# Kernel optimization log

Measured on AMD Instinct MI355X. Metric: run time of the kernel, lower is better.

## Reference

```python
import jax, jax.numpy as jnp
import numpy as np

B, DX, DY = 128, 3, 3
D = DX * DY          # max_digit = 9
N = D * D            # num_nodes = 81
HID = 96
EMB = 16
ITERS = 4
M = B * N * D        # LSTM flattened rows = 93312


def _sudoku_adj():
    idx = np.arange(N)
    r, c = idx // D, idx % D
    br, bc = r // DX, c // DY
    same = (r[:, None] == r[None]) | (c[:, None] == c[None]) | ((br[:, None] == br[None]) & (bc[:, None] == bc[None]))
    return (same & ~np.eye(N, dtype=bool)).astype(np.float32)


def setup_inputs() -> dict:
    key = jax.random.key(0)
    ks = iter(jax.random.split(key, 40))

    def dense(shape, fan_in):
        return jax.random.normal(next(ks), shape, jnp.float32) / np.float32(np.sqrt(fan_in))

    return {
        "inputs": jax.random.randint(next(ks), (B, N), 0, D + 1, jnp.int32),
        "c0": jax.random.normal(next(ks), (M, HID), jnp.float32),
        "adj_cell": jnp.asarray((np.ones((D, D)) - np.eye(D)).astype(np.float32)),
        "adj_digit": jnp.asarray(_sudoku_adj()),
        "enc_W1": dense((3, EMB), 3), "enc_b1": jnp.zeros((EMB,), jnp.float32),
        "enc_W2": dense((EMB, HID), EMB), "enc_b2": jnp.zeros((HID,), jnp.float32),
        "cr_W": dense((3, HID, HID), HID), "cr_b": jnp.zeros((3, HID), jnp.float32),
        "dr_W": dense((3, HID, HID), HID), "dr_b": jnp.zeros((3, HID), jnp.float32),
        "gm_W1": dense((3 * HID, HID), 3 * HID), "gm_b1": jnp.zeros((HID,), jnp.float32),
        "gm_W2": dense((2, HID, HID), HID), "gm_b2": jnp.zeros((2, HID), jnp.float32),
        "lstm_Wih": dense((4 * HID, HID), HID), "lstm_Whh": dense((4 * HID, HID), HID),
        "lstm_bih": jnp.zeros((4 * HID,), jnp.float32), "lstm_bhh": jnp.zeros((4 * HID,), jnp.float32),
        "r_W12": dense((2, HID, HID), HID), "r_b12": jnp.zeros((2, HID), jnp.float32),
        "r_W3": dense((HID, 1), HID), "r_b3": jnp.zeros((1,), jnp.float32),
        "iters": ITERS,
    }


def _mlp(x, Ws, bs):
    # stacked MLP: ReLU between layers, none after the last
    L = Ws.shape[0]
    for l in range(L):
        x = x @ Ws[l] + bs[l]
        if l < L - 1:
            x = jax.nn.relu(x)
    return x


def _forward(inputs, c0, adj_cell, adj_digit, enc_W1, enc_b1, enc_W2, enc_b2,
             cr_W, cr_b, dr_W, dr_b, gm_W1, gm_b1, gm_W2, gm_b2,
             lstm_Wih, lstm_Whh, lstm_bih, lstm_bhh, r_W12, r_b12, r_W3, r_b3, iters):
    # mask: [B,N,D,3] = (blank, equals digit d+1, filled-with-other-digit)
    eq = inputs[:, :, None] == jnp.arange(1, D + 1, dtype=inputs.dtype)[None, None, :]
    given = inputs != 0
    mask = jnp.stack([
        jnp.broadcast_to((~given)[:, :, None], eq.shape), eq,
        (~eq) & given[:, :, None]
    ], axis=-1).astype(jnp.float32)

    X = jax.nn.relu(mask @ enc_W1 + enc_b1) @ enc_W2 + enc_b2  # [B,N,D,HID]

    def lstm_step(x, h, c):
        gates = x @ lstm_Wih.T + lstm_bih + h @ lstm_Whh.T + lstm_bhh
        i, f, g, o = jnp.split(gates, 4, axis=-1)  # PyTorch gate order i,f,g,o
        c = jax.nn.sigmoid(f) * c + jax.nn.sigmoid(i) * jnp.tanh(g)
        h = jax.nn.sigmoid(o) * jnp.tanh(c)
        return h, c

    def step(carry, _):
        h, c = carry  # [M,HID] each
        Hn = h.reshape(X.shape)
        # relational message passing: per-node MLP then sum over graph edges
        msg_cell = jnp.einsum('bndh,de->bneh', _mlp(Hn, cr_W, cr_b), adj_cell)
        msg_digit = jnp.einsum('bndh,nm->bmdh', _mlp(Hn, dr_W, dr_b), adj_digit)
        g = jnp.concatenate([X, msg_cell, msg_digit], axis=-1)  # [B,N,D,3*HID]
        g = jax.nn.relu(g @ gm_W1 + gm_b1)
        g = jax.nn.relu(g @ gm_W2[0] + gm_b2[0])
        g = g @ gm_W2[1] + gm_b2[1]
        h, c = lstm_step(g.reshape(-1, HID), h, c)
        Hn = h.reshape(X.shape)
        out = jax.nn.relu(Hn @ r_W12[0] + r_b12[0])
        out = jax.nn.relu(out @ r_W12[1] + r_b12[1])
        out = (out @ r_W3 + r_b3)[..., 0]  # [B,N,D]
        return (h, c), out

    (_, _), outs = jax.lax.scan(step, (X.reshape(-1, HID), c0), None, length=iters)
    return outs  # [iters,B,N,D]


def reference(inputs, c0, adj_cell, adj_digit, enc_W1, enc_b1, enc_W2, enc_b2,
              cr_W, cr_b, dr_W, dr_b, gm_W1, gm_b1, gm_W2, gm_b2,
              lstm_Wih, lstm_Whh, lstm_bih, lstm_bhh, r_W12, r_b12, r_W3, r_b3, iters):
    return _forward(inputs, c0, adj_cell, adj_digit, enc_W1, enc_b1, enc_W2, enc_b2,
                    cr_W, cr_b, dr_W, dr_b, gm_W1, gm_b1, gm_W2, gm_b2,
                    lstm_Wih, lstm_Whh, lstm_bih, lstm_bhh, r_W12, r_b12, r_W3, r_b3, iters)
```

## Files before the change

kernel.cpp:

```cpp
#include <hip/hip_runtime.h>
#include <hip/hip_bf16.h>

typedef unsigned short u16;
typedef __bf16 bf16x8 __attribute__((ext_vector_type(8)));
typedef float  f32x4  __attribute__((ext_vector_type(4)));
typedef u16    u16x8  __attribute__((ext_vector_type(8)));

#define HID   96
#define LDP   104
#define MROWS 93312
#define BN    10368
#define GRID_TILE 1458
#define FUSE_GRID 5832
#define SGS   104
#define PST   97

#define FCH 9216

#define MFMA(a,b,c) __builtin_amdgcn_mfma_f32_16x16x32_bf16((a),(b),(c),0,0,0)

__device__ __forceinline__ float bf2f(u16 x){
  union { float f; unsigned u; } v; v.u = ((unsigned)x) << 16; return v.f;
}
__device__ __forceinline__ u16 f2bf(float f){
  union { float f; unsigned u; } v; v.f = f;
  unsigned r = v.u + 0x7fffu + ((v.u >> 16) & 1u);
  return (u16)(r >> 16);
}
__device__ __forceinline__ float frcp(float x){ return __builtin_amdgcn_rcpf(x); }
__device__ __forceinline__ float sigf(float x){ return frcp(1.f + __expf(-x)); }
__device__ __forceinline__ float tanhf_(float x){
  float xx = fminf(fmaxf(x, -15.f), 15.f);
  float e = __expf(-2.f * xx);
  return (1.f - e) * frcp(1.f + e);
}
__device__ __forceinline__ void lds_fence(){
  asm volatile("s_waitcnt lgkmcnt(0)" ::: "memory");
}

struct Frags { bf16x8 a0, a1, a2; };

__device__ __forceinline__ Frags load_afrags_g(const u16* __restrict__ A, size_t row0, int lane){
  int t16 = lane & 15, q = lane >> 4;
  const u16* p = A + (row0 + (size_t)t16) * 96 + q * 8;
  Frags f;
  f.a0 = *reinterpret_cast<const bf16x8*>(p);
  f.a1 = *reinterpret_cast<const bf16x8*>(p + 32);
  f.a2 = *reinterpret_cast<const bf16x8*>(p + 64);
  return f;
}
__device__ __forceinline__ Frags load_afrags_s(const u16* sA, int row0, int lane){
  int t16 = lane & 15, q = lane >> 4;
  const u16* p = sA + (row0 + t16) * LDP + q * 8;
  Frags f;
  f.a0 = *reinterpret_cast<const bf16x8*>(p);
  f.a1 = *reinterpret_cast<const bf16x8*>(p + 32);
  f.a2 = *reinterpret_cast<const bf16x8*>(p + 64);
  return f;
}

__device__ __forceinline__ void layer_g(Frags f, const u16* __restrict__ wb,
    const float* __restrict__ bias, u16* dst, int dstStride, size_t rowBase,
    bool relu, int lane)
{
  int t16 = lane & 15, q = lane >> 4;
  #pragma unroll
  for (int nt = 0; nt < 6; nt++){
    float b = bias ? bias[nt * 16 + t16] : 0.f;
    f32x4 acc = {b, b, b, b};
    const u16* wp = wb + nt * 1536 + lane * 8;
    acc = MFMA(f.a0, *reinterpret_cast<const bf16x8*>(wp),        acc);
    acc = MFMA(f.a1, *reinterpret_cast<const bf16x8*>(wp + 512),  acc);
    acc = MFMA(f.a2, *reinterpret_cast<const bf16x8*>(wp + 1024), acc);
    #pragma unroll
    for (int j = 0; j < 4; j++){
      float v = acc[j];
      if (relu) v = fmaxf(v, 0.f);
      dst[(rowBase + q * 4 + j) * (size_t)dstStride + nt * 16 + t16] = f2bf(v);
    }
  }
}

__device__ __forceinline__ void layer_split(Frags f, const u16* __restrict__ wb,
    const float* __restrict__ bias, u16* dst, bool relu, int lane, int w)
{
  int t16 = lane & 15, q = lane >> 4;
  #pragma unroll
  for (int nt = w; nt < 6; nt += 4){
    float b = bias ? bias[nt * 16 + t16] : 0.f;
    f32x4 acc = {b, b, b, b};
    const u16* wp = wb + nt * 1536 + lane * 8;
    acc = MFMA(f.a0, *reinterpret_cast<const bf16x8*>(wp),        acc);
    acc = MFMA(f.a1, *reinterpret_cast<const bf16x8*>(wp + 512),  acc);
    acc = MFMA(f.a2, *reinterpret_cast<const bf16x8*>(wp + 1024), acc);
    #pragma unroll
    for (int j = 0; j < 4; j++){
      float v = acc[j];
      if (relu) v = fmaxf(v, 0.f);
      dst[(q * 4 + j) * LDP + nt * 16 + t16] = f2bf(v);
    }
  }
}

__device__ __forceinline__ void mfma6_g(f32x4* acc, Frags f,
    const u16* __restrict__ wb, int lane)
{
  #pragma unroll
  for (int jt = 0; jt < 6; jt++){
    const u16* wp = wb + jt * 1536 + lane * 8;
    acc[jt] = MFMA(f.a0, *reinterpret_cast<const bf16x8*>(wp),        acc[jt]);
    acc[jt] = MFMA(f.a1, *reinterpret_cast<const bf16x8*>(wp + 512),  acc[jt]);
    acc[jt] = MFMA(f.a2, *reinterpret_cast<const bf16x8*>(wp + 1024), acc[jt]);
  }
}

__global__ __launch_bounds__(256) void k_prep2(const float* __restrict__ crW,
    const float* __restrict__ drW, const float* __restrict__ gmW2,
    const float* __restrict__ rW12, const float* __restrict__ Whh,
    u16* __restrict__ pWB)
{
  int b = blockIdx.x, tid = threadIdx.x;
  if (b < 7){
    const float* src; int ch;
    if      (b == 0){ src = crW;          ch = 0;  }
    else if (b == 1){ src = crW  + 9216;  ch = 1;  }
    else if (b == 2){ src = drW;          ch = 3;  }
    else if (b == 3){ src = drW  + 9216;  ch = 4;  }
    else if (b == 4){ src = gmW2;         ch = 8;  }
    else if (b == 5){ src = rW12;         ch = 10; }
    else            { src = rW12 + 9216;  ch = 11; }
    u16* dst = pWB + ch * FCH;
    #pragma unroll
    for (int i = 0; i < 36; i++){
      int idx = tid + i * 256;
      int f = idx >> 9, rem = idx & 511, l = rem >> 3, j = rem & 7;
      int nt = f / 3, kc = f - nt * 3;
      int n = nt * 16 + (l & 15);
      int k = ((l >> 4) << 3) + kc * 32 + j;
      dst[idx] = f2bf(src[k * 96 + n]);
    }
  } else {
    int bb = b - 7;
    u16* dst = pWB + (16 + bb) * FCH;
    const float* src = Whh + bb * 9216;
    #pragma unroll
    for (int i = 0; i < 36; i++){
      int idx = tid + i * 256;
      int f = idx >> 9, rem = idx & 511, l = rem >> 3, j = rem & 7;
      int nt = f / 3, kc = f - nt * 3;
      int n = nt * 16 + (l & 15);
      int k = ((l >> 4) << 3) + kc * 32 + j;
      dst[idx] = f2bf(src[n * 96 + k]);
    }
  }
}

__global__ __launch_bounds__(256) void k_prepc(const float* __restrict__ crW,
    const float* __restrict__ crB, const float* __restrict__ drW,
    const float* __restrict__ drB, const float* __restrict__ gmW1,
    u16* __restrict__ pWB, float* __restrict__ bY, float* __restrict__ bZ)
{
  __shared__ float sM[96 * PST];
  __shared__ float sW[96 * PST];
  int b = blockIdx.x, g = b / 9, seg = b - g * 9, tid = threadIdx.x;
  const float* L = (g == 0 ? crW : drW) + 2 * 9216;
  const float* R = gmW1 + (g == 0 ? 9216 : 18432);
  for (int i = tid; i < 9216; i += 256){
    int r = i / 96, cc = i - r * 96;
    sM[r * PST + cc] = L[i];
    sW[r * PST + cc] = R[i];
  }
  __syncthreads();
  if (seg == 0){
    const float* bv = (g == 0 ? crB : drB) + 192;
    float* bo = (g == 0 ? bY : bZ);
    for (int n = tid; n < 96; n += 256){
      float a = 0.f;
      for (int j = 0; j < 96; j++) a += bv[j] * sW[j * PST + n];
      bo[n] = a;
    }
  }
  u16* dst = pWB + (g == 0 ? 2 : 5) * FCH;
  #pragma unroll
  for (int i = 0; i < 4; i++){
    int idx = seg * 1024 + tid + i * 256;
    int f = idx >> 9, rem = idx & 511, l = rem >> 3, j = rem & 7;
    int nt = f / 3, kc = f - nt * 3;
    int n = nt * 16 + (l & 15);
    int k = ((l >> 4) << 3) + kc * 32 + j;
    float a = 0.f;
    #pragma unroll 4
    for (int jj = 0; jj < 96; jj++) a += sM[k * PST + jj] * sW[jj * PST + n];
    dst[idx] = f2bf(a);
  }
}

__global__ __launch_bounds__(256) void k_prepf(const float* __restrict__ gmW2,
    const float* __restrict__ Wih, u16* __restrict__ pWB)
{
  __shared__ float sW[96 * PST];
  int b = blockIdx.x, g = b / 9, seg = b - g * 9, tid = threadIdx.x;
  for (int i = tid; i < 9216; i += 256){
    int r = i / 96, cc = i - r * 96;
    sW[r * PST + cc] = gmW2[9216 + i];
  }
  __syncthreads();
  u16* dst = pWB + (12 + g) * FCH;
  #pragma unroll
  for (int i = 0; i < 4; i++){
    int idx = seg * 1024 + tid + i * 256;
    int f = idx >> 9, rem = idx & 511, l = rem >> 3, j = rem & 7;
    int nt = f / 3, kc = f - nt * 3;
    int n = nt * 16 + (l & 15);
    int k = ((l >> 4) << 3) + kc * 32 + j;
    const float* wr = Wih + (g * 96 + n) * 96;
    float a = 0.f;
    #pragma unroll 4
    for (int jj = 0; jj < 96; jj++) a += sW[k * PST + jj] * wr[jj];
    dst[idx] = f2bf(a);
  }
}

__global__ void k_tables(const float* __restrict__ eW1, const float* __restrict__ eb1,
                         const float* __restrict__ eW2, const float* __restrict__ eb2,
                         const float* __restrict__ gmW1, const float* __restrict__ gmb1,
                         const float* __restrict__ bih, const float* __restrict__ bhh,
                         const float* __restrict__ gmb2, const float* __restrict__ Wih,
                         float* __restrict__ XTab, float* __restrict__ XgTab,
                         float* __restrict__ bsx)
{
  __shared__ float sX[3][96];
  int j = threadIdx.x;
  for (int n = j; n < 384; n += 128){
    float acc = bih[n] + bhh[n];
    const float* wr = Wih + n * 96;
    for (int jj = 0; jj < 96; jj++) acc += gmb2[96 + jj] * wr[jj];
    bsx[n] = acc;
  }
  if (j < 96){
    for (int ch = 0; ch < 3; ch++){
      float acc = eb2[j];
      for (int e = 0; e < 16; e++){
        float hv = fmaxf(eW1[ch * 16 + e] + eb1[e], 0.f);
        acc += hv * eW2[e * 96 + j];
      }
      sX[ch][j] = acc;
      XTab[ch * 96 + j] = acc;
    }
  }
  __syncthreads();
  if (j < 96){
    for (int ch = 0; ch < 3; ch++){
      float acc = gmb1[j];
      for (int k = 0; k < 96; k++) acc += sX[ch][k] * gmW1[k * 96 + j];
      XgTab[ch * 96 + j] = acc;
    }
  }
}

__global__ __launch_bounds__(256) void k_init(const int* __restrict__ inputs,
    const float* __restrict__ XTab, u16* __restrict__ h)
{
  int idx = blockIdx.x * 256 + threadIdx.x;
  int m = idx / 12, h8 = idx - m * 12;
  int bn = m / 9, d = m - bn * 9;
  int inp = inputs[bn];
  int ch = (inp == 0) ? 0 : ((inp == d + 1) ? 1 : 2);
  const float* xt = XTab + ch * 96 + h8 * 8;
  u16* hp = h + (size_t)m * 96 + h8 * 8;
  #pragma unroll
  for (int e = 0; e < 8; e++) hp[e] = f2bf(xt[e]);
}

__global__ __launch_bounds__(256) void k_ab3(const u16* __restrict__ h,
    u16* __restrict__ Y, u16* __restrict__ Z,
    const u16* __restrict__ pWB, const float* __restrict__ crB,
    const float* __restrict__ drB, const float* __restrict__ bY,
    const float* __restrict__ bZ)
{
  __shared__ u16 sA[64 * LDP];
  const int tid = threadIdx.x, lane = tid & 63, wave = tid >> 6;
  const int wrow = wave * 16;
  const size_t rbase = (size_t)blockIdx.x * 64;

  Frags hf = load_afrags_g(h, rbase + wrow, lane);

  layer_g(hf, pWB, crB, sA, LDP, wrow, true, lane);                  lds_fence();
  Frags f = load_afrags_s(sA, wrow, lane);
  layer_g(f, pWB + 1 * FCH, crB + 96, sA, LDP, wrow, true, lane);    lds_fence();
  f = load_afrags_s(sA, wrow, lane);
  layer_g(f, pWB + 2 * FCH, bY, Y, 96, rbase + wrow, false, lane);
  lds_fence();

  layer_g(hf, pWB + 3 * FCH, drB, sA, LDP, wrow, true, lane);        lds_fence();
  f = load_afrags_s(sA, wrow, lane);
  layer_g(f, pWB + 4 * FCH, drB + 96, sA, LDP, wrow, true, lane);    lds_fence();
  f = load_afrags_s(sA, wrow, lane);
  layer_g(f, pWB + 5 * FCH, bZ, Z, 96, rbase + wrow, false, lane);
}

__device__ __forceinline__ void addrow(float* s, const u16* p){
  u16x8 t = *reinterpret_cast<const u16x8*>(p);
  #pragma unroll
  for (int e = 0; e < 8; e++) s[e] += bf2f(t[e]);
}

__global__ __launch_bounds__(256) void k_msg(u16* __restrict__ Z,
    const u16* __restrict__ Y, u16* __restrict__ Ssum)
{
  __shared__ u16 sT[81 * LDP];
  const int tid = threadIdx.x;
  if (blockIdx.x >= 1152){
    int idx = (blockIdx.x - 1152) * 256 + tid;
    int bn = idx / 12, h8 = idx - bn * 12;
    const u16* base = Y + (size_t)bn * 864 + h8 * 8;
    float s[8];
    #pragma unroll
    for (int e = 0; e < 8; e++) s[e] = 0.f;
    #pragma unroll
    for (int d = 0; d < 9; d++){
      u16x8 v = *reinterpret_cast<const u16x8*>(base + d * 96);
      #pragma unroll
      for (int e = 0; e < 8; e++) s[e] += bf2f(v[e]);
    }
    u16x8 o;
    #pragma unroll
    for (int e = 0; e < 8; e++) o[e] = f2bf(s[e]);
    *reinterpret_cast<u16x8*>(Ssum + (size_t)bn * 96 + h8 * 8) = o;
    return;
  }
  const int b = blockIdx.x / 9, d = blockIdx.x - b * 9;
  const size_t base = ((size_t)b * 729 + d) * 96;
  for (int i = tid; i < 972; i += 256){
    int n = i / 12, k8 = i - n * 12;
    *reinterpret_cast<u16x8*>(sT + n * LDP + k8 * 8) =
      *reinterpret_cast<const u16x8*>(Z + base + (size_t)n * 864 + k8 * 8);
  }
  __syncthreads();
  for (int i = tid; i < 972; i += 256){
    int m = i / 12, k8 = i - m * 12;
    int r = m / 9, cc = m - r * 9;
    int br = (r / 3) * 3, bc = (cc / 3) * 3;
    float s[8];
    #pragma unroll
    for (int e = 0; e < 8; e++) s[e] = 0.f;
    #pragma unroll
    for (int c2 = 0; c2 < 9; c2++) if (c2 != cc) addrow(s, sT + (r * 9 + c2) * LDP + k8 * 8);
    #pragma unroll
    for (int r2 = 0; r2 < 9; r2++) if (r2 != r) addrow(s, sT + (r2 * 9 + cc) * LDP + k8 * 8);
    #pragma unroll
    for (int r2 = 0; r2 < 3; r2++)
      #pragma unroll
      for (int c2 = 0; c2 < 3; c2++){
        int rr = br + r2, c3 = bc + c2;
        if (rr != r && c3 != cc) addrow(s, sT + (rr * 9 + c3) * LDP + k8 * 8);
      }
    u16x8 o;
    #pragma unroll
    for (int e = 0; e < 8; e++) o[e] = f2bf(s[e]);
    *reinterpret_cast<u16x8*>(Z + base + (size_t)m * 864 + k8 * 8) = o;
  }
}

__global__ __launch_bounds__(256, 4) void k_fuse16(const u16* __restrict__ Y,
    const u16* __restrict__ Zd, const u16* __restrict__ Ssum,
    const int* __restrict__ inputs, const float* __restrict__ XgTab,
    const u16* __restrict__ pWB, const float* __restrict__ gmb2,
    u16* h, const float* cin, float* cout,
    const float* __restrict__ bsx, const float* __restrict__ rb12,
    const float* __restrict__ rW3, const float* __restrict__ rb3,
    float* __restrict__ out)
{
  __shared__ u16 sA[16 * LDP];
  __shared__ u16 sB[16 * LDP];
  __shared__ float sG[4][16][SGS];
  const int tid = threadIdx.x, lane = tid & 63, w = tid >> 6;
  const int t16 = lane & 15, q = lane >> 4;
  const size_t rbase = (size_t)blockIdx.x * 16;

  float cpre[6];
  #pragma unroll
  for (int e = 0; e < 6; e++){
    int idx = e * 256 + tid;
    int r = idx / 96, col = idx - r * 96;
    cpre[e] = cin[(rbase + r) * 96 + col];
  }
  Frags fh = load_afrags_g(h, rbase, lane);

  if (tid < 192){
    int rl = tid / 12, kc = tid - rl * 12;
    int m = (int)rbase + rl;
    int bn = m / 9, d = m - bn * 9;
    int inp = inputs[bn];
    int ch = (inp == 0) ? 0 : ((inp == d + 1) ? 1 : 2);
    const float* xg = XgTab + ch * 96 + kc * 8;
    u16x8 vy = *reinterpret_cast<const u16x8*>(Y    + (size_t)m * 96 + kc * 8);
    u16x8 vz = *reinterpret_cast<const u16x8*>(Zd   + (size_t)m * 96 + kc * 8);
    u16x8 vs = *reinterpret_cast<const u16x8*>(Ssum + (size_t)bn * 96 + kc * 8);
    u16x8 o;
    #pragma unroll
    for (int e = 0; e < 8; e++)
      o[e] = f2bf(fmaxf(xg[e] + bf2f(vs[e]) - bf2f(vy[e]) + bf2f(vz[e]), 0.f));
    *reinterpret_cast<u16x8*>(sA + rl * LDP + kc * 8) = o;
  }
  __syncthreads();

  {
    Frags f = load_afrags_s(sA, 0, lane);
    layer_split(f, pWB + 8 * FCH, gmb2, sB, true, lane, w);
  }
  __syncthreads();

  f32x4 acc[6];
  #pragma unroll
  for (int nt = 0; nt < 6; nt++){
    float b = bsx[w * 96 + nt * 16 + t16];
    f32x4 a = {b, b, b, b};
    acc[nt] = a;
  }
  {
    Frags fa = load_afrags_s(sB, 0, lane);
    mfma6_g(acc, fa, pWB + (12 + w) * FCH, lane);
    mfma6_g(acc, fh, pWB + (16 + w) * FCH, lane);
  }
  #pragma unroll
  for (int nt = 0; nt < 6; nt++)
    #pragma unroll
    for (int j = 0; j < 4; j++)
      sG[w][q * 4 + j][nt * 16 + t16] = acc[nt][j];
  __syncthreads();

  #pragma unroll
  for (int e = 0; e < 6; e++){
    int idx = e * 256 + tid;
    int r = idx / 96, col = idx - r * 96;
    float iv = sG[0][r][col];
    float fv = sG[1][r][col];
    float gv = sG[2][r][col];
    float ov = sG[3][r][col];
    size_t m = rbase + r;
    float cn = sigf(fv) * cpre[e] + sigf(iv) * tanhf_(gv);
    float hn = sigf(ov) * tanhf_(cn);
    cout[m * 96 + col] = cn;
    u16 hb = f2bf(hn);
    h[m * 96 + col] = hb;
    sA[r * LDP + col] = hb;
  }
  __syncthreads();

  {
    Frags f = load_afrags_s(sA, 0, lane);
    layer_split(f, pWB + 10 * FCH, rb12, sB, true, lane, w);
  }
  __syncthreads();
  {
    Frags f = load_afrags_s(sB, 0, lane);
    layer_split(f, pWB + 11 * FCH, rb12 + 96, sA, true, lane, w);
  }
  __syncthreads();

  if (tid < 64){
    int row = tid >> 2, part = tid & 3;
    float s = 0.f;
    const u16* rp = sA + row * LDP + part * 24;
    #pragma unroll
    for (int k = 0; k < 24; k++) s += bf2f(rp[k]) * rW3[part * 24 + k];
    s += __shfl_xor(s, 1);
    s += __shfl_xor(s, 2);
    if (part == 0) out[rbase + row] = s + rb3[0];
  }
}

extern "C" void kernel_launch(void* const* d_in, const int* in_sizes, int n_in,
                              void* d_out, int out_size, void* d_ws, size_t ws_size,
                              hipStream_t stream)
{
  (void)in_sizes; (void)n_in; (void)out_size; (void)ws_size;
  const int*   inputs = (const int*)d_in[0];
  const float* c0     = (const float*)d_in[1];
  const float* eW1  = (const float*)d_in[4];
  const float* eb1  = (const float*)d_in[5];
  const float* eW2  = (const float*)d_in[6];
  const float* eb2  = (const float*)d_in[7];
  const float* crW  = (const float*)d_in[8];
  const float* crB  = (const float*)d_in[9];
  const float* drW  = (const float*)d_in[10];
  const float* drB  = (const float*)d_in[11];
  const float* gmW1 = (const float*)d_in[12];
  const float* gmb1 = (const float*)d_in[13];
  const float* gmW2 = (const float*)d_in[14];
  const float* gmb2 = (const float*)d_in[15];
  const float* Wih  = (const float*)d_in[16];
  const float* Whh  = (const float*)d_in[17];
  const float* bih  = (const float*)d_in[18];
  const float* bhh  = (const float*)d_in[19];
  const float* rW12 = (const float*)d_in[20];
  const float* rb12 = (const float*)d_in[21];
  const float* rW3  = (const float*)d_in[22];
  const float* rb3  = (const float*)d_in[23];

  char* ws = (char*)d_ws;
  float* XgTab = (float*)(ws);
  float* XTab  = (float*)(ws + 4096);
  float* bsx   = (float*)(ws + 6144);
  float* bY    = (float*)(ws + 7680);
  float* bZ    = (float*)(ws + 8064);
  u16*   pWB   = (u16*)(ws + 8704);
  u16* h  = (u16*)(ws + 409600);
  u16* B1 = h  + (size_t)MROWS * 96;
  u16* B2 = B1 + (size_t)MROWS * 96;
  float* c = (float*)(B2 + (size_t)MROWS * 96);
  u16* Ssum = (u16*)(c + (size_t)MROWS * 96);
  float* out = (float*)d_out;

  k_prep2<<<11, 256, 0, stream>>>(crW, drW, gmW2, rW12, Whh, pWB);
  k_prepc<<<18, 256, 0, stream>>>(crW, crB, drW, drB, gmW1, pWB, bY, bZ);
  k_prepf<<<36, 256, 0, stream>>>(gmW2, Wih, pWB);
  k_tables<<<1, 128, 0, stream>>>(eW1, eb1, eW2, eb2, gmW1, gmb1, bih, bhh,
                                  gmb2, Wih, XTab, XgTab, bsx);
  k_init<<<(MROWS * 12) / 256, 256, 0, stream>>>(inputs, XTab, h);

  for (int it = 0; it < 4; ++it){
    const float* cin = (it == 0) ? c0 : c;
    k_ab3<<<GRID_TILE, 256, 0, stream>>>(h, B1, B2, pWB, crB, drB, bY, bZ);
    k_msg<<<1152 + 486, 256, 0, stream>>>(B2, B1, Ssum);
    k_fuse16<<<FUSE_GRID, 256, 0, stream>>>(B1, B2, Ssum, inputs, XgTab, pWB,
                                            gmb2, h, cin, c, bsx, rb12, rW3, rb3,
                                            out + (size_t)it * MROWS);
  }
}
```

Before: 676.4 us.

## Fuse next iteration's cell/digit MLPs into the LSTM fuse kernel tail

Moves the k_ab3 work (the two 3-layer MLPs producing Y and Z for the next iteration) into the end of k_fuse16x, which already holds the new h tile in shared memory. This drops one kernel launch per iteration and avoids re-reading h from global memory. k_ab3 now runs only once before the loop. The change reuses the sG buffer as extra bf16 scratch, which shrinks its stride and may add bank conflicts. It also lengthens the fuse kernel, which may raise register pressure and lower occupancy. Y and Z are overwritten in place after being read earlier in the same block, which is safe only because each block touches only its own rows.

After: 661.0 us. 1.02x faster.

```diff
diff --git a/kernel.cpp b/kernel.cpp
--- a/kernel.cpp
+++ b/kernel.cpp
@@ -12,7 +12,7 @@
 #define BN    10368
 #define GRID_TILE 1458
 #define FUSE_GRID 5832
-#define SGS   104
+#define SGX   100
 #define PST   97
 
 #define FCH 9216
@@ -98,6 +98,27 @@
       float v = acc[j];
       if (relu) v = fmaxf(v, 0.f);
       dst[(q * 4 + j) * LDP + nt * 16 + t16] = f2bf(v);
+    }
+  }
+}
+
+__device__ __forceinline__ void layer_split_gout(Frags f, const u16* __restrict__ wb,
+    const float* __restrict__ bias, u16* gdst, size_t rbase, bool relu, int lane, int w)
+{
+  int t16 = lane & 15, q = lane >> 4;
+  #pragma unroll
+  for (int nt = w; nt < 6; nt += 4){
+    float b = bias ? bias[nt * 16 + t16] : 0.f;
+    f32x4 acc = {b, b, b, b};
+    const u16* wp = wb + nt * 1536 + lane * 8;
+    acc = MFMA(f.a0, *reinterpret_cast<const bf16x8*>(wp),        acc);
+    acc = MFMA(f.a1, *reinterpret_cast<const bf16x8*>(wp + 512),  acc);
+    acc = MFMA(f.a2, *reinterpret_cast<const bf16x8*>(wp + 1024), acc);
+    #pragma unroll
+    for (int j = 0; j < 4; j++){
+      float v = acc[j];
+      if (relu) v = fmaxf(v, 0.f);
+      gdst[(rbase + q * 4 + j) * 96 + nt * 16 + t16] = f2bf(v);
     }
   }
 }
@@ -362,18 +383,21 @@
   }
 }
 
-__global__ __launch_bounds__(256, 4) void k_fuse16(const u16* __restrict__ Y,
-    const u16* __restrict__ Zd, const u16* __restrict__ Ssum,
+__global__ __launch_bounds__(256, 4) void k_fuse16x(u16* Y, u16* Z,
+    const u16* __restrict__ Ssum,
     const int* __restrict__ inputs, const float* __restrict__ XgTab,
     const u16* __restrict__ pWB, const float* __restrict__ gmb2,
     u16* h, const float* cin, float* cout,
     const float* __restrict__ bsx, const float* __restrict__ rb12,
     const float* __restrict__ rW3, const float* __restrict__ rb3,
-    float* __restrict__ out)
+    float* __restrict__ out, const float* __restrict__ crB,
+    const float* __restrict__ drB, const float* __restrict__ bY,
+    const float* __restrict__ bZ, int doAB)
 {
   __shared__ u16 sA[16 * LDP];
   __shared__ u16 sB[16 * LDP];
-  __shared__ float sG[4][16][SGS];
+  __shared__ float sG[4][16][SGX];
+  u16* sC = reinterpret_cast<u16*>(sG);
   const int tid = threadIdx.x, lane = tid & 63, w = tid >> 6;
   const int t16 = lane & 15, q = lane >> 4;
   const size_t rbase = (size_t)blockIdx.x * 16;
@@ -395,7 +419,7 @@
     int ch = (inp == 0) ? 0 : ((inp == d + 1) ? 1 : 2);
     const float* xg = XgTab + ch * 96 + kc * 8;
     u16x8 vy = *reinterpret_cast<const u16x8*>(Y    + (size_t)m * 96 + kc * 8);
-    u16x8 vz = *reinterpret_cast<const u16x8*>(Zd   + (size_t)m * 96 + kc * 8);
+    u16x8 vz = *reinterpret_cast<const u16x8*>(Z    + (size_t)m * 96 + kc * 8);
     u16x8 vs = *reinterpret_cast<const u16x8*>(Ssum + (size_t)bn * 96 + kc * 8);
     u16x8 o;
     #pragma unroll
@@ -455,19 +479,47 @@
   __syncthreads();
   {
     Frags f = load_afrags_s(sB, 0, lane);
-    layer_split(f, pWB + 11 * FCH, rb12 + 96, sA, true, lane, w);
+    layer_split(f, pWB + 11 * FCH, rb12 + 96, sC, true, lane, w);
   }
   __syncthreads();
 
   if (tid < 64){
     int row = tid >> 2, part = tid & 3;
     float s = 0.f;
-    const u16* rp = sA + row * LDP + part * 24;
+    const u16* rp = sC + row * LDP + part * 24;
     #pragma unroll
     for (int k = 0; k < 24; k++) s += bf2f(rp[k]) * rW3[part * 24 + k];
     s += __shfl_xor(s, 1);
     s += __shfl_xor(s, 2);
     if (part == 0) out[rbase + row] = s + rb3[0];
+  }
+  if (doAB){
+    {
+      Frags f = load_afrags_s(sA, 0, lane);
+      layer_split(f, pWB + 0 * FCH, crB, sB, true, lane, w);
+    }
+    __syncthreads();
+    {
+      Frags f = load_afrags_s(sB, 0, lane);
+      layer_split(f, pWB + 1 * FCH, crB + 96, sC, true, lane, w);
+    }
+    __syncthreads();
+    {
+      Frags f = load_afrags_s(sC, 0, lane);
+      layer_split_gout(f, pWB + 2 * FCH, bY, Y, rbase, false, lane, w);
+      Frags f2 = load_afrags_s(sA, 0, lane);
+      layer_split(f2, pWB + 3 * FCH, drB, sB, true, lane, w);
+    }
+    __syncthreads();
+    {
+      Frags f = load_afrags_s(sB, 0, lane);
+      layer_split(f, pWB + 4 * FCH, drB + 96, sC, true, lane, w);
+    }
+    __syncthreads();
+    {
+      Frags f = load_afrags_s(sC, 0, lane);
+      layer_split_gout(f, pWB + 5 * FCH, bZ, Z, rbase, false, lane, w);
+    }
   }
 }
 
@@ -519,13 +571,14 @@
   k_tables<<<1, 128, 0, stream>>>(eW1, eb1, eW2, eb2, gmW1, gmb1, bih, bhh,
                                   gmb2, Wih, XTab, XgTab, bsx);
   k_init<<<(MROWS * 12) / 256, 256, 0, stream>>>(inputs, XTab, h);
+  k_ab3<<<GRID_TILE, 256, 0, stream>>>(h, B1, B2, pWB, crB, drB, bY, bZ);
 
   for (int it = 0; it < 4; ++it){
     const float* cin = (it == 0) ? c0 : c;
-    k_ab3<<<GRID_TILE, 256, 0, stream>>>(h, B1, B2, pWB, crB, drB, bY, bZ);
     k_msg<<<1152 + 486, 256, 0, stream>>>(B2, B1, Ssum);
-    k_fuse16<<<FUSE_GRID, 256, 0, stream>>>(B1, B2, Ssum, inputs, XgTab, pWB,
-                                            gmb2, h, cin, c, bsx, rb12, rW3, rb3,
-                                            out + (size_t)it * MROWS);
-  }
-}
+    k_fuse16x<<<FUSE_GRID, 256, 0, stream>>>(B1, B2, Ssum, inputs, XgTab, pWB,
+                                             gmb2, h, cin, c, bsx, rb12, rW3, rb3,
+                                             out + (size_t)it * MROWS,
+                                             crB, drB, bY, bZ, (it < 3) ? 1 : 0);
+  }
+}
```
